# Kernel optimization log

Hardware: AMD Instinct MI355X
Metric: run time of the kernel (lower is better)

## Reference

```python
import jax, jax.numpy as jnp
import numpy as np

NUM_HEADS = 16
THRESHOLD = 4e-4  # < 1/S so every softmax row keeps >=1 entry (classical path of grover_search_filter)


def setup_inputs() -> dict:
    key = jax.random.key(0)
    k0, k1, k2 = jax.random.split(key, 3)
    B, S, E = 4, 1024, 1024
    x = jax.random.normal(k0, (B, S, E), dtype=jnp.float32)
    Wqkv = jax.random.normal(k1, (3 * E, E), dtype=jnp.float32) * 0.02
    bqkv = jnp.zeros((3 * E,), dtype=jnp.float32)
    Wproj = jax.random.normal(k2, (E, E), dtype=jnp.float32) * 0.02
    bproj = jnp.zeros((E,), dtype=jnp.float32)
    return {"x": x, "Wqkv": Wqkv, "bqkv": bqkv, "Wproj": Wproj, "bproj": bproj}


def reference(x, Wqkv, bqkv, Wproj, bproj):
    B, S, E = x.shape
    H = NUM_HEADS
    D = E // H
    scale = D ** -0.5
    # qkv projection -> (3, B, H, S, D), matching torch permute(2,0,3,1,4)
    qkv = (x @ Wqkv.T + bqkv).reshape(B, S, 3, H, D).transpose(2, 0, 3, 1, 4)
    q, k, v = qkv[0], qkv[1], qkv[2]
    attn_logits = jnp.einsum("bhqd,bhkd->bhqk", q, k) * scale  # [B,H,S,S]
    attn_probs = jax.nn.softmax(attn_logits, axis=-1)
    # grover_search_filter: seq_len > 2**max_qubits -> classical threshold mask
    selected = attn_probs > THRESHOLD
    filtered_logits = jnp.where(selected, attn_logits, -jnp.inf)
    filtered_attn = jax.nn.softmax(filtered_logits, axis=-1)
    # dropout is identity in eval mode
    out = jnp.einsum("bhqk,bhkd->bhqd", filtered_attn, v)
    out = out.transpose(0, 2, 1, 3).reshape(B, S, E)
    out = out @ Wproj.T + bproj
    return out, filtered_attn
```

## Files before the change

kernel.cpp:

```cpp
#include <hip/hip_runtime.h>
#include <hip/hip_bf16.h>
#include <cstdint>


#define BB 4
#define SS 1024
#define EE 1024
#define HH 16
#define DD 64

typedef __attribute__((ext_vector_type(8))) short bf16x8;
typedef __attribute__((ext_vector_type(4))) float f32x4;

__global__ __launch_bounds__(256) void split_w(
    const float* __restrict__ Wqkv, const float* __restrict__ Wproj,
    __hip_bfloat16* __restrict__ Wqh, __hip_bfloat16* __restrict__ Wql,
    __hip_bfloat16* __restrict__ Wph) {
  int i = blockIdx.x * 256 + threadIdx.x;
  const int NQ4 = 768 * 1024;
  if (i < NQ4) {
    float4 v = ((const float4*)Wqkv)[i];
    float vv[4] = {v.x, v.y, v.z, v.w};
    __hip_bfloat16 h[4], l[4];
#pragma unroll
    for (int j = 0; j < 4; ++j) {
      h[j] = __float2bfloat16(vv[j]);
      l[j] = __float2bfloat16(vv[j] - __bfloat162float(h[j]));
    }
    ((ushort4*)Wqh)[i] = *(ushort4*)h;
    ((ushort4*)Wql)[i] = *(ushort4*)l;
  } else {
    int j4 = i - NQ4;
    float4 v = ((const float4*)Wproj)[j4];
    __hip_bfloat16 h[4];
    h[0] = __float2bfloat16(v.x); h[1] = __float2bfloat16(v.y);
    h[2] = __float2bfloat16(v.z); h[3] = __float2bfloat16(v.w);
    ((ushort4*)Wph)[j4] = *(ushort4*)h;
  }
}

__global__ __launch_bounds__(256) void gemm_qkv(
    const float* __restrict__ X, const __hip_bfloat16* __restrict__ Wh,
    const __hip_bfloat16* __restrict__ Wl, const float* __restrict__ bias,
    __hip_bfloat16* __restrict__ o1, __hip_bfloat16* __restrict__ o2,
    __hip_bfloat16* __restrict__ o3, __hip_bfloat16* __restrict__ o4,
    __hip_bfloat16* __restrict__ o5, int M) {
  const int tid  = threadIdx.x;
  const int lane = tid & 63;
  const int wave = tid >> 6;
  const int wm   = (wave >> 1) * 64;
  const int wn   = (wave & 1) * 64;
  const int quad = lane >> 4;
  const int l15  = lane & 15;
  const int m0   = blockIdx.y * 128;
  const int n0   = blockIdx.x * 128;

  __shared__ __align__(16) __hip_bfloat16 lAh[128 * 72];
  __shared__ __align__(16) __hip_bfloat16 lAl[128 * 72];

  f32x4 acc[4][4] = {};
  const __hip_bfloat16* pBh = Wh + (long long)(n0 + wn + l15) * 1024 + quad * 8;
  const __hip_bfloat16* pBl = Wl + (long long)(n0 + wn + l15) * 1024 + quad * 8;

  for (int k0 = 0; k0 < 1024; k0 += 64) {
#pragma unroll
    for (int it = 0; it < 4; ++it) {
      int flat = (it * 256 + tid) * 8;
      int row  = flat >> 6;
      int kk   = flat & 63;
      const float* src = X + (long long)(m0 + row) * 1024 + k0 + kk;
      float4 f0 = *(const float4*)src;
      float4 f1 = *(const float4*)(src + 4);
      float vv[8] = {f0.x, f0.y, f0.z, f0.w, f1.x, f1.y, f1.z, f1.w};
      __hip_bfloat16 t[8], u[8];
#pragma unroll
      for (int j2 = 0; j2 < 8; ++j2) {
        t[j2] = __float2bfloat16(vv[j2]);
        u[j2] = __float2bfloat16(vv[j2] - __bfloat162float(t[j2]));
      }
      *(uint4*)&lAh[row * 72 + kk] = *(uint4*)t;
      *(uint4*)&lAl[row * 72 + kk] = *(uint4*)u;
    }
    __syncthreads();

#pragma unroll
    for (int ks = 0; ks < 64; ks += 32) {
      bf16x8 ah[4], al[4], bh[4], bl[4];
#pragma unroll
      for (int i = 0; i < 4; ++i) {
        int off = (wm + i * 16 + l15) * 72 + ks + quad * 8;
        ah[i] = *(const bf16x8*)&lAh[off];
        al[i] = *(const bf16x8*)&lAl[off];
      }
#pragma unroll
      for (int j = 0; j < 4; ++j) {
        const long long boff = (long long)j * 16 * 1024 + k0 + ks;
        bh[j] = *(const bf16x8*)(pBh + boff);
        bl[j] = *(const bf16x8*)(pBl + boff);
      }
#pragma unroll
      for (int i = 0; i < 4; ++i)
#pragma unroll
        for (int j = 0; j < 4; ++j) {
          acc[i][j] = __builtin_amdgcn_mfma_f32_16x16x32_bf16(al[i], bh[j], acc[i][j], 0, 0, 0);
          acc[i][j] = __builtin_amdgcn_mfma_f32_16x16x32_bf16(ah[i], bl[j], acc[i][j], 0, 0, 0);
          acc[i][j] = __builtin_amdgcn_mfma_f32_16x16x32_bf16(ah[i], bh[j], acc[i][j], 0, 0, 0);
        }
    }
    __syncthreads();
  }

#pragma unroll
  for (int i = 0; i < 4; ++i) {
#pragma unroll
    for (int j = 0; j < 4; ++j) {
#pragma unroll
      for (int r = 0; r < 4; ++r) {
        int m = m0 + wm + i * 16 + quad * 4 + r;
        int n = n0 + wn + j * 16 + l15;
        float v = acc[i][j][r] + bias[n];
        int c = n >> 10, nn = n & 1023, h = nn >> 6, d = nn & 63;
        int b = m >> 10, s = m & 1023;
        long long idx = (((long long)(b * HH + h) * SS + s) << 6) + d;
        if (c == 0) {
          v *= 0.125f;
          __hip_bfloat16 hh = __float2bfloat16(v);
          o1[idx] = hh;
          o2[idx] = __float2bfloat16(v - __bfloat162float(hh));
        } else if (c == 1) {
          __hip_bfloat16 hh = __float2bfloat16(v);
          o3[idx] = hh;
          o4[idx] = __float2bfloat16(v - __bfloat162float(hh));
        } else {
          o5[(((long long)(b * HH + h) * DD + d) << 10) + s] = __float2bfloat16(v);
        }
      }
    }
  }
}

__global__ __launch_bounds__(256) void gemm_out(
    const __hip_bfloat16* __restrict__ Ah, const __hip_bfloat16* __restrict__ Bh,
    const float* __restrict__ bias, float* __restrict__ oF, int M) {
  const int tid  = threadIdx.x;
  const int lane = tid & 63;
  const int wave = tid >> 6;
  const int wm   = (wave >> 1) * 64;
  const int wn   = (wave & 1) * 64;
  const int quad = lane >> 4;
  const int l15  = lane & 15;
  const int m0   = blockIdx.y * 128;
  const int n0   = blockIdx.x * 128;

  __shared__ __align__(16) __hip_bfloat16 lds[2 * 128 * 72];
  __hip_bfloat16* lA = lds;
  __hip_bfloat16* lB = lds + 128 * 72;

  f32x4 acc[4][4] = {};

  for (int k0 = 0; k0 < 1024; k0 += 64) {
#pragma unroll
    for (int it = 0; it < 4; ++it) {
      int flat = (it * 256 + tid) * 8;
      int row  = flat >> 6;
      int kk   = flat & 63;
      uint4 va = *(const uint4*)(Ah + (long long)(m0 + row) * 1024 + k0 + kk);
      *(uint4*)&lA[row * 72 + kk] = va;
      uint4 vb = *(const uint4*)(Bh + (long long)(n0 + row) * 1024 + k0 + kk);
      *(uint4*)&lB[row * 72 + kk] = vb;
    }
    __syncthreads();

#pragma unroll
    for (int ks = 0; ks < 64; ks += 32) {
      bf16x8 ah[4], bh[4];
#pragma unroll
      for (int i = 0; i < 4; ++i)
        ah[i] = *(const bf16x8*)&lA[(wm + i * 16 + l15) * 72 + ks + quad * 8];
#pragma unroll
      for (int j = 0; j < 4; ++j)
        bh[j] = *(const bf16x8*)&lB[(wn + j * 16 + l15) * 72 + ks + quad * 8];
#pragma unroll
      for (int i = 0; i < 4; ++i)
#pragma unroll
        for (int j = 0; j < 4; ++j)
          acc[i][j] = __builtin_amdgcn_mfma_f32_16x16x32_bf16(ah[i], bh[j], acc[i][j], 0, 0, 0);
    }
    __syncthreads();
  }

#pragma unroll
  for (int i = 0; i < 4; ++i)
#pragma unroll
    for (int j = 0; j < 4; ++j)
#pragma unroll
      for (int r = 0; r < 4; ++r) {
        int m = m0 + wm + i * 16 + quad * 4 + r;
        int n = n0 + wn + j * 16 + l15;
        oF[(long long)m * EE + n] = acc[i][j][r] + bias[n];
      }
}

__device__ __forceinline__ float qg_max16(float v) {
#pragma unroll
  for (int o = 8; o > 0; o >>= 1) v = fmaxf(v, __shfl_xor(v, o));
  return v;
}
__device__ __forceinline__ float qg_sum16(float v) {
#pragma unroll
  for (int o = 8; o > 0; o >>= 1) v += __shfl_xor(v, o);
  return v;
}

__global__ __launch_bounds__(512, 4) void fused_attn(
    const __hip_bfloat16* __restrict__ qh, const __hip_bfloat16* __restrict__ ql,
    const __hip_bfloat16* __restrict__ kh, const __hip_bfloat16* __restrict__ kl,
    const __hip_bfloat16* __restrict__ vT, float* __restrict__ attn,
    __hip_bfloat16* __restrict__ ao) {
  const int tid  = threadIdx.x;
  const int lane = tid & 63;
  const int wave = tid >> 6;
  const int quad = lane >> 4;
  const int l15  = lane & 15;

  int id = blockIdx.x;
  const int q8 = gridDim.x >> 3;
  id = (id & 7) * q8 + (id >> 3);
  const int bh = id >> 5;
  const int q0 = (id & 31) * 32;

  const int brow = (bh >> 4) * SS;
  const int h    = bh & 15;
  const long long qbase = ((long long)bh * SS + q0) * DD;
  const long long kbase = (long long)bh * SS * DD;
  const long long vbase = (long long)bh * DD * SS;
  const long long abase = ((long long)bh * SS + q0) * SS;

  __shared__ __align__(16) __hip_bfloat16 Pl[32][1032];
  __shared__ float red[3][8][32];
  __shared__ float Obuf[4][32][17];

  bf16x8 aqh0[2], aqh1[2], aql0[2], aql1[2];
#pragma unroll
  for (int s = 0; s < 2; ++s) {
    const __hip_bfloat16* ph = qh + qbase + (s * 16 + l15) * DD + quad * 8;
    const __hip_bfloat16* pl = ql + qbase + (s * 16 + l15) * DD + quad * 8;
    aqh0[s] = *(const bf16x8*)(ph);
    aqh1[s] = *(const bf16x8*)(ph + 32);
    aql0[s] = *(const bf16x8*)(pl);
    aql1[s] = *(const bf16x8*)(pl + 32);
  }

  f32x4 acc0[8], acc1[8];
  const __hip_bfloat16* pkh0 = kh + kbase + (long long)(wave * 128 + l15) * DD + quad * 8;
  const __hip_bfloat16* pkl0 = kl + kbase + (long long)(wave * 128 + l15) * DD + quad * 8;
#pragma unroll
  for (int nt = 0; nt < 8; ++nt) {
    const __hip_bfloat16* pkh = pkh0 + nt * 16 * DD;
    const __hip_bfloat16* pkl = pkl0 + nt * 16 * DD;
    f32x4 a0 = {}, a1 = {};
    {
      bf16x8 b = *(const bf16x8*)(pkh);
      bf16x8 c = *(const bf16x8*)(pkl);
      __builtin_amdgcn_s_setprio(1);
      a0 = __builtin_amdgcn_mfma_f32_16x16x32_bf16(aql0[0], b, a0, 0, 0, 0);
      a1 = __builtin_amdgcn_mfma_f32_16x16x32_bf16(aql0[1], b, a1, 0, 0, 0);
      a0 = __builtin_amdgcn_mfma_f32_16x16x32_bf16(aqh0[0], c, a0, 0, 0, 0);
      a1 = __builtin_amdgcn_mfma_f32_16x16x32_bf16(aqh0[1], c, a1, 0, 0, 0);
      a0 = __builtin_amdgcn_mfma_f32_16x16x32_bf16(aqh0[0], b, a0, 0, 0, 0);
      a1 = __builtin_amdgcn_mfma_f32_16x16x32_bf16(aqh0[1], b, a1, 0, 0, 0);
      __builtin_amdgcn_s_setprio(0);
    }
    {
      bf16x8 b = *(const bf16x8*)(pkh + 32);
      bf16x8 c = *(const bf16x8*)(pkl + 32);
      __builtin_amdgcn_s_setprio(1);
      a0 = __builtin_amdgcn_mfma_f32_16x16x32_bf16(aql1[0], b, a0, 0, 0, 0);
      a1 = __builtin_amdgcn_mfma_f32_16x16x32_bf16(aql1[1], b, a1, 0, 0, 0);
      a0 = __builtin_amdgcn_mfma_f32_16x16x32_bf16(aqh1[0], c, a0, 0, 0, 0);
      a1 = __builtin_amdgcn_mfma_f32_16x16x32_bf16(aqh1[1], c, a1, 0, 0, 0);
      a0 = __builtin_amdgcn_mfma_f32_16x16x32_bf16(aqh1[0], b, a0, 0, 0, 0);
      a1 = __builtin_amdgcn_mfma_f32_16x16x32_bf16(aqh1[1], b, a1, 0, 0, 0);
      __builtin_amdgcn_s_setprio(0);
    }
    acc0[nt] = a0;
    acc1[nt] = a1;
  }

  {
    float mx0[4], mx1[4];
#pragma unroll
    for (int r = 0; r < 4; ++r) {
      float a = fmaxf(fmaxf(fmaxf(acc0[0][r], acc0[1][r]), fmaxf(acc0[2][r], acc0[3][r])),
                      fmaxf(fmaxf(acc0[4][r], acc0[5][r]), fmaxf(acc0[6][r], acc0[7][r])));
      mx0[r] = qg_max16(a);
      float b = fmaxf(fmaxf(fmaxf(acc1[0][r], acc1[1][r]), fmaxf(acc1[2][r], acc1[3][r])),
                      fmaxf(fmaxf(acc1[4][r], acc1[5][r]), fmaxf(acc1[6][r], acc1[7][r])));
      mx1[r] = qg_max16(b);
    }
    if (l15 == 0) {
#pragma unroll
      for (int r = 0; r < 4; ++r) {
        red[0][wave][quad * 4 + r]      = mx0[r];
        red[0][wave][16 + quad * 4 + r] = mx1[r];
      }
    }
  }
  __syncthreads();
  float m0[4], m1[4];
#pragma unroll
  for (int r = 0; r < 4; ++r) {
    const int q = quad * 4 + r;
    m0[r] = fmaxf(fmaxf(fmaxf(red[0][0][q], red[0][1][q]), fmaxf(red[0][2][q], red[0][3][q])),
                  fmaxf(fmaxf(red[0][4][q], red[0][5][q]), fmaxf(red[0][6][q], red[0][7][q])));
    m1[r] = fmaxf(fmaxf(fmaxf(red[0][0][16 + q], red[0][1][16 + q]), fmaxf(red[0][2][16 + q], red[0][3][16 + q])),
                  fmaxf(fmaxf(red[0][4][16 + q], red[0][5][16 + q]), fmaxf(red[0][6][16 + q], red[0][7][16 + q])));
  }

  {
    float z0[4] = {0.f, 0.f, 0.f, 0.f}, z1[4] = {0.f, 0.f, 0.f, 0.f};
#pragma unroll
    for (int nt = 0; nt < 8; ++nt)
#pragma unroll
      for (int r = 0; r < 4; ++r) {
        float e0 = expf(acc0[nt][r] - m0[r]);
        acc0[nt][r] = e0; z0[r] += e0;
        float e1 = expf(acc1[nt][r] - m1[r]);
        acc1[nt][r] = e1; z1[r] += e1;
      }
#pragma unroll
    for (int r = 0; r < 4; ++r) { z0[r] = qg_sum16(z0[r]); z1[r] = qg_sum16(z1[r]); }
    if (l15 == 0) {
#pragma unroll
      for (int r = 0; r < 4; ++r) {
        red[1][wave][quad * 4 + r]      = z0[r];
        red[1][wave][16 + quad * 4 + r] = z1[r];
      }
    }
  }
  __syncthreads();
  float c0[4], c1[4];
#pragma unroll
  for (int r = 0; r < 4; ++r) {
    const int q = quad * 4 + r;
    const float Z0 = ((red[1][0][q] + red[1][1][q]) + (red[1][2][q] + red[1][3][q])) +
                     ((red[1][4][q] + red[1][5][q]) + (red[1][6][q] + red[1][7][q]));
    const float Z1 = ((red[1][0][16 + q] + red[1][1][16 + q]) + (red[1][2][16 + q] + red[1][3][16 + q])) +
                     ((red[1][4][16 + q] + red[1][5][16 + q]) + (red[1][6][16 + q] + red[1][7][16 + q]));
    c0[r] = 4e-4f * Z0;
    c1[r] = 4e-4f * Z1;
  }

  {
    float s0[4] = {0.f, 0.f, 0.f, 0.f}, s1[4] = {0.f, 0.f, 0.f, 0.f};
#pragma unroll
    for (int nt = 0; nt < 8; ++nt)
#pragma unroll
      for (int r = 0; r < 4; ++r) {
        if (acc0[nt][r] > c0[r]) s0[r] += acc0[nt][r];
        if (acc1[nt][r] > c1[r]) s1[r] += acc1[nt][r];
      }
#pragma unroll
    for (int r = 0; r < 4; ++r) { s0[r] = qg_sum16(s0[r]); s1[r] = qg_sum16(s1[r]); }
    if (l15 == 0) {
#pragma unroll
      for (int r = 0; r < 4; ++r) {
        red[2][wave][quad * 4 + r]      = s0[r];
        red[2][wave][16 + quad * 4 + r] = s1[r];
      }
    }
  }
  __syncthreads();
  float rinv0[4], rinv1[4];
#pragma unroll
  for (int r = 0; r < 4; ++r) {
    const int q = quad * 4 + r;
    const float Zs0 = ((red[2][0][q] + red[2][1][q]) + (red[2][2][q] + red[2][3][q])) +
                      ((red[2][4][q] + red[2][5][q]) + (red[2][6][q] + red[2][7][q]));
    const float Zs1 = ((red[2][0][16 + q] + red[2][1][16 + q]) + (red[2][2][16 + q] + red[2][3][16 + q])) +
                      ((red[2][4][16 + q] + red[2][5][16 + q]) + (red[2][6][16 + q] + red[2][7][16 + q]));
    rinv0[r] = 1.0f / Zs0;
    rinv1[r] = 1.0f / Zs1;
  }

#pragma unroll
  for (int nt = 0; nt < 8; ++nt) {
    const int k = wave * 128 + nt * 16 + l15;
#pragma unroll
    for (int r = 0; r < 4; ++r) {
      const int q = quad * 4 + r;
      const float e0 = acc0[nt][r];
      const float p0 = (e0 > c0[r]) ? e0 * rinv0[r] : 0.f;
      attn[abase + (long long)q * SS + k] = p0;
      Pl[q][k] = __float2bfloat16(p0);
      const float e1 = acc1[nt][r];
      const float p1 = (e1 > c1[r]) ? e1 * rinv1[r] : 0.f;
      attn[abase + (long long)(16 + q) * SS + k] = p1;
      Pl[16 + q][k] = __float2bfloat16(p1);
    }
  }
  __syncthreads();

  const int d0  = (wave & 3) * 16;
  const int kh2 = (wave >> 2) * 512;
  f32x4 oA0 = {}, oA1 = {}, oB0 = {}, oB1 = {};
  const __hip_bfloat16* pv  = vT + vbase + (long long)(d0 + l15) * SS + kh2 + quad * 8;
  const __hip_bfloat16* pp0 = &Pl[l15][kh2] + quad * 8;
  const __hip_bfloat16* pp1 = &Pl[16 + l15][kh2] + quad * 8;
#pragma unroll
  for (int ks = 0; ks < 16; ks += 2) {
    bf16x8 v0  = *(const bf16x8*)(pv + ks * 32);
    bf16x8 v1  = *(const bf16x8*)(pv + (ks + 1) * 32);
    bf16x8 a00 = *(const bf16x8*)(pp0 + ks * 32);
    bf16x8 a01 = *(const bf16x8*)(pp0 + (ks + 1) * 32);
    bf16x8 a10 = *(const bf16x8*)(pp1 + ks * 32);
    bf16x8 a11 = *(const bf16x8*)(pp1 + (ks + 1) * 32);
    __builtin_amdgcn_s_setprio(1);
    oA0 = __builtin_amdgcn_mfma_f32_16x16x32_bf16(a00, v0, oA0, 0, 0, 0);
    oB0 = __builtin_amdgcn_mfma_f32_16x16x32_bf16(a10, v0, oB0, 0, 0, 0);
    oA1 = __builtin_amdgcn_mfma_f32_16x16x32_bf16(a01, v1, oA1, 0, 0, 0);
    oB1 = __builtin_amdgcn_mfma_f32_16x16x32_bf16(a11, v1, oB1, 0, 0, 0);
    __builtin_amdgcn_s_setprio(0);
  }
  float oS0[4], oS1[4];
#pragma unroll
  for (int r = 0; r < 4; ++r) { oS0[r] = oA0[r] + oA1[r]; oS1[r] = oB0[r] + oB1[r]; }

  if (wave >= 4) {
#pragma unroll
    for (int r = 0; r < 4; ++r) {
      Obuf[wave & 3][quad * 4 + r][l15]      = oS0[r];
      Obuf[wave & 3][16 + quad * 4 + r][l15] = oS1[r];
    }
  }
  __syncthreads();
  if (wave < 4) {
#pragma unroll
    for (int r = 0; r < 4; ++r) {
      const int qA = q0 + quad * 4 + r;
      const int qB = qA + 16;
      const float vA = oS0[r] + Obuf[wave][quad * 4 + r][l15];
      const float vB = oS1[r] + Obuf[wave][16 + quad * 4 + r][l15];
      ao[((long long)(brow + qA)) * EE + h * DD + d0 + l15] = __float2bfloat16(vA);
      ao[((long long)(brow + qB)) * EE + h * DD + d0 + l15] = __float2bfloat16(vB);
    }
  }
}

extern "C" void kernel_launch(void* const* d_in, const int* in_sizes, int n_in,
                              void* d_out, int out_size, void* d_ws, size_t ws_size,
                              hipStream_t stream) {
  const float* x     = (const float*)d_in[0];
  const float* Wqkv  = (const float*)d_in[1];
  const float* bqkv  = (const float*)d_in[2];
  const float* Wproj = (const float*)d_in[3];
  const float* bproj = (const float*)d_in[4];

  float* out   = (float*)d_out;
  float* attnF = out + (size_t)BB * SS * EE;

  const size_t M1 = 1024 * 1024;
  __hip_bfloat16* w = (__hip_bfloat16*)d_ws;

  if (ws_size >= (size_t)80 * 1024 * 1024) {
    __hip_bfloat16 *Wqh = w, *Wql = Wqh + 3 * M1, *Wph = Wql + 3 * M1;
    __hip_bfloat16 *qh = Wph + M1, *ql = qh + 4 * M1, *kh = ql + 4 * M1, *kl = kh + 4 * M1;
    __hip_bfloat16 *vT = kl + 4 * M1, *ao = vT + 4 * M1;

    split_w<<<4096, 256, 0, stream>>>(Wqkv, Wproj, Wqh, Wql, Wph);
    gemm_qkv<<<dim3(24, 32), 256, 0, stream>>>(
        x, Wqh, Wql, bqkv, qh, ql, kh, kl, vT, 4096);
    fused_attn<<<dim3(BB * HH * 32), 512, 0, stream>>>(
        qh, ql, kh, kl, vT, attnF, ao);
    gemm_out<<<dim3(8, 32), 256, 0, stream>>>(ao, Wph, bproj, out, 4096);
    return;
  }

  __hip_bfloat16 *Wqh = w, *Wql = Wqh + 3 * M1, *Wph = Wql + 3 * M1;
  __hip_bfloat16 *qh = Wph + M1, *ql = qh + M1, *kh = ql + M1, *kl = kh + M1;
  __hip_bfloat16 *vT = kl + M1, *ao = vT + M1;

  split_w<<<4096, 256, 0, stream>>>(Wqkv, Wproj, Wqh, Wql, Wph);

  for (int b = 0; b < BB; ++b) {
    const float* xb   = x + (size_t)b * SS * EE;
    float* attnb      = attnF + (size_t)b * HH * SS * SS;
    float* outb       = out + (size_t)b * SS * EE;

    gemm_qkv<<<dim3(24, 8), 256, 0, stream>>>(
        xb, Wqh, Wql, bqkv, qh, ql, kh, kl, vT, 1024);
    fused_attn<<<dim3(HH * 32), 512, 0, stream>>>(
        qh, ql, kh, kl, vT, attnb, ao);
    gemm_out<<<dim3(8, 8), 256, 0, stream>>>(ao, Wph, bproj, outb, 1024);
  }
}
```

Before: 649.9 us.

## Write unnormalized P to LDS early and apply row normalization after PV

```diff
diff --git a/kernel.cpp b/kernel.cpp
--- a/kernel.cpp
+++ b/kernel.cpp
@@ -238,7 +238,6 @@
 
   __shared__ __align__(16) __hip_bfloat16 Pl[32][1032];
   __shared__ float red[3][8][32];
-  __shared__ float Obuf[4][32][17];
 
   bf16x8 aqh0[2], aqh1[2], aql0[2], aql1[2];
 #pragma unroll
@@ -370,7 +369,20 @@
       }
     }
   }
+#pragma unroll
+  for (int nt = 0; nt < 8; ++nt) {
+    const int k = wave * 128 + nt * 16 + l15;
+#pragma unroll
+    for (int r = 0; r < 4; ++r) {
+      const int q = quad * 4 + r;
+      const float e0 = acc0[nt][r];
+      Pl[q][k]      = (e0 > c0[r]) ? __float2bfloat16(e0) : __float2bfloat16(0.f);
+      const float e1 = acc1[nt][r];
+      Pl[16 + q][k] = (e1 > c1[r]) ? __float2bfloat16(e1) : __float2bfloat16(0.f);
+    }
+  }
   __syncthreads();
+
   float rinv0[4], rinv1[4];
 #pragma unroll
   for (int r = 0; r < 4; ++r) {
@@ -390,60 +402,34 @@
     for (int r = 0; r < 4; ++r) {
       const int q = quad * 4 + r;
       const float e0 = acc0[nt][r];
-      const float p0 = (e0 > c0[r]) ? e0 * rinv0[r] : 0.f;
-      attn[abase + (long long)q * SS + k] = p0;
-      Pl[q][k] = __float2bfloat16(p0);
+      attn[abase + (long long)q * SS + k]        = (e0 > c0[r]) ? e0 * rinv0[r] : 0.f;
       const float e1 = acc1[nt][r];
-      const float p1 = (e1 > c1[r]) ? e1 * rinv1[r] : 0.f;
-      attn[abase + (long long)(16 + q) * SS + k] = p1;
-      Pl[16 + q][k] = __float2bfloat16(p1);
-    }
-  }
-  __syncthreads();
-
-  const int d0  = (wave & 3) * 16;
-  const int kh2 = (wave >> 2) * 512;
-  f32x4 oA0 = {}, oA1 = {}, oB0 = {}, oB1 = {};
-  const __hip_bfloat16* pv  = vT + vbase + (long long)(d0 + l15) * SS + kh2 + quad * 8;
-  const __hip_bfloat16* pp0 = &Pl[l15][kh2] + quad * 8;
-  const __hip_bfloat16* pp1 = &Pl[16 + l15][kh2] + quad * 8;
-#pragma unroll
-  for (int ks = 0; ks < 16; ks += 2) {
-    bf16x8 v0  = *(const bf16x8*)(pv + ks * 32);
-    bf16x8 v1  = *(const bf16x8*)(pv + (ks + 1) * 32);
-    bf16x8 a00 = *(const bf16x8*)(pp0 + ks * 32);
-    bf16x8 a01 = *(const bf16x8*)(pp0 + (ks + 1) * 32);
-    bf16x8 a10 = *(const bf16x8*)(pp1 + ks * 32);
-    bf16x8 a11 = *(const bf16x8*)(pp1 + (ks + 1) * 32);
+      attn[abase + (long long)(16 + q) * SS + k] = (e1 > c1[r]) ? e1 * rinv1[r] : 0.f;
+    }
+  }
+
+  const int st = wave & 1;
+  const int d0 = (wave >> 1) * 16;
+  f32x4 o0 = {}, o1 = {};
+  const __hip_bfloat16* pv = vT + vbase + (long long)(d0 + l15) * SS + quad * 8;
+  const __hip_bfloat16* pp = &Pl[st * 16 + l15][0] + quad * 8;
+#pragma unroll
+  for (int ks = 0; ks < 32; ks += 2) {
+    bf16x8 a0 = *(const bf16x8*)(pp + ks * 32);
+    bf16x8 v0 = *(const bf16x8*)(pv + ks * 32);
+    bf16x8 a1 = *(const bf16x8*)(pp + (ks + 1) * 32);
+    bf16x8 v1 = *(const bf16x8*)(pv + (ks + 1) * 32);
     __builtin_amdgcn_s_setprio(1);
-    oA0 = __builtin_amdgcn_mfma_f32_16x16x32_bf16(a00, v0, oA0, 0, 0, 0);
-    oB0 = __builtin_amdgcn_mfma_f32_16x16x32_bf16(a10, v0, oB0, 0, 0, 0);
-    oA1 = __builtin_amdgcn_mfma_f32_16x16x32_bf16(a01, v1, oA1, 0, 0, 0);
-    oB1 = __builtin_amdgcn_mfma_f32_16x16x32_bf16(a11, v1, oB1, 0, 0, 0);
+    o0 = __builtin_amdgcn_mfma_f32_16x16x32_bf16(a0, v0, o0, 0, 0, 0);
+    o1 = __builtin_amdgcn_mfma_f32_16x16x32_bf16(a1, v1, o1, 0, 0, 0);
     __builtin_amdgcn_s_setprio(0);
   }
-  float oS0[4], oS1[4];
-#pragma unroll
-  for (int r = 0; r < 4; ++r) { oS0[r] = oA0[r] + oA1[r]; oS1[r] = oB0[r] + oB1[r]; }
-
-  if (wave >= 4) {
-#pragma unroll
-    for (int r = 0; r < 4; ++r) {
-      Obuf[wave & 3][quad * 4 + r][l15]      = oS0[r];
-      Obuf[wave & 3][16 + quad * 4 + r][l15] = oS1[r];
-    }
-  }
-  __syncthreads();
-  if (wave < 4) {
-#pragma unroll
-    for (int r = 0; r < 4; ++r) {
-      const int qA = q0 + quad * 4 + r;
-      const int qB = qA + 16;
-      const float vA = oS0[r] + Obuf[wave][quad * 4 + r][l15];
-      const float vB = oS1[r] + Obuf[wave][16 + quad * 4 + r][l15];
-      ao[((long long)(brow + qA)) * EE + h * DD + d0 + l15] = __float2bfloat16(vA);
-      ao[((long long)(brow + qB)) * EE + h * DD + d0 + l15] = __float2bfloat16(vB);
-    }
+#pragma unroll
+  for (int r = 0; r < 4; ++r) {
+    const float rv = st ? rinv1[r] : rinv0[r];
+    const float v  = (o0[r] + o1[r]) * rv;
+    const int q = q0 + st * 16 + quad * 4 + r;
+    ao[((long long)(brow + q)) * EE + h * DD + d0 + l15] = __float2bfloat16(v);
   }
 }
 
```

After: 646.6 us. About the same (-0.5%).
